# Kernel optimization log

Measured on AMD Instinct MI355X. Metric: run time of the kernel, lower is better.

The kernel has to match this reference:

```python
import jax, jax.numpy as jnp
import numpy as np

B, S, D, H, DK, DV = 2, 2048, 1024, 16, 64, 64


def setup_inputs() -> dict:
    key = jax.random.key(0)
    ks = jax.random.split(key, 12)
    inp = {
        "query": jax.random.normal(ks[0], (B, S, D), jnp.float32),
        "key":   jax.random.normal(ks[1], (B, S, D), jnp.float32),
        "value": jax.random.normal(ks[2], (B, S, D), jnp.float32),
        # additive mask broadcast over per-head [B,S,S] scores (zeros = no masking)
        "mask":  jnp.zeros((S, S), jnp.float32),
        # stacked per-head projection params (math-equivalent to H separate Linears)
        "Wq": jax.random.normal(ks[3], (H, D, DK), jnp.float32) / np.sqrt(D),
        "bq": jax.random.normal(ks[4], (H, DK), jnp.float32) * 0.02,
        "Wk": jax.random.normal(ks[5], (H, D, DK), jnp.float32) / np.sqrt(D),
        "bk": jax.random.normal(ks[6], (H, DK), jnp.float32) * 0.02,
        "Wv": jax.random.normal(ks[7], (H, D, DV), jnp.float32) / np.sqrt(D),
        "bv": jax.random.normal(ks[8], (H, DV), jnp.float32) * 0.02,
        "Wo": jax.random.normal(ks[9], (H * DV, D), jnp.float32) / np.sqrt(H * DV),
        "bo": jax.random.normal(ks[10], (D,), jnp.float32) * 0.02,
    }
    return inp


def reference(query, key, value, mask, Wq, bq, Wk, bk, Wv, bv, Wo, bo):
    # per-head projections, vectorized over heads
    q = jnp.einsum("bsd,hdk->bhsk", query, Wq) + bq[None, :, None, :]
    k = jnp.einsum("bsd,hdk->bhsk", key, Wk) + bk[None, :, None, :]
    v = jnp.einsum("bsd,hdv->bhsv", value, Wv) + bv[None, :, None, :]
    # explicit QK^T softmax V, scale by sqrt(dim_k) (key.size(-1))
    scores = jnp.einsum("bhsk,bhtk->bhst", q, k) / jnp.sqrt(jnp.asarray(DK, q.dtype))
    scores = scores + mask  # broadcast [S,S] -> [B,H,S,S]
    attn = jax.nn.softmax(scores, axis=-1)
    out = jnp.einsum("bhst,bhtv->bhsv", attn, v)
    # concat heads along last dim: [B,S,H*DV]
    out = out.transpose(0, 2, 1, 3).reshape(B, S, H * DV)
    return out @ Wo + bo
```

## Files before the change

### kernel.cpp

```cpp
#include <hip/hip_runtime.h>
#include <stdint.h>

typedef __bf16 bf16;
typedef float f32x4 __attribute__((ext_vector_type(4)));
typedef __bf16 bf16x8 __attribute__((ext_vector_type(8)));
typedef __bf16 bf16x4 __attribute__((ext_vector_type(4)));
typedef __bf16 bf16x2 __attribute__((ext_vector_type(2)));
typedef unsigned u32x2 __attribute__((ext_vector_type(2)));
typedef unsigned u32x4 __attribute__((ext_vector_type(4)));

__device__ __forceinline__ void async_load16(const void* g, void* l) {
    __builtin_amdgcn_global_load_lds(
        (const __attribute__((address_space(1))) void*)g,
        (__attribute__((address_space(3))) void*)l, 16, 0, 0);
}

__device__ __forceinline__ unsigned pk2(float lo, float hi) {
    bf16x2 t;
    t[0] = (bf16)lo;
    t[1] = (bf16)hi;
    return __builtin_bit_cast(unsigned, t);
}

#if __has_builtin(__builtin_amdgcn_permlane32_swap)
#define PLSWAP32(A_, B_) do { u32x2 _r = __builtin_amdgcn_permlane32_swap((A_), (B_), false, false); (A_) = _r[0]; (B_) = _r[1]; } while (0)
#else
#define PLSWAP32(A_, B_) asm("v_permlane32_swap_b32 %0, %1" : "+v"(A_), "+v"(B_))
#endif
#if __has_builtin(__builtin_amdgcn_permlane16_swap)
#define PLSWAP16(A_, B_) do { u32x2 _r = __builtin_amdgcn_permlane16_swap((A_), (B_), false, false); (A_) = _r[0]; (B_) = _r[1]; } while (0)
#else
#define PLSWAP16(A_, B_) asm("v_permlane16_swap_b32 %0, %1" : "+v"(A_), "+v"(B_))
#endif

__global__ void detect_dtype(const unsigned short* __restrict__ q, int* __restrict__ flag) {
    __shared__ int cnt;
    if (threadIdx.x == 0) cnt = 0;
    __syncthreads();
    int c = 0;
    for (int i = threadIdx.x; i < 4096; i += 256) {
        int e = (q[i] >> 7) & 0xFF;
        if (e >= 0xC0) ++c;
    }
    atomicAdd(&cnt, c);
    __syncthreads();
    if (threadIdx.x == 0) { flag[0] = (cnt > 64) ? 1 : 0; flag[1] = 0; }
}

__global__ void prep(const void* __restrict__ qv, const void* __restrict__ vv,
                     const void* __restrict__ kvraw,
                     const void* __restrict__ wq, const void* __restrict__ wk,
                     const void* __restrict__ wv, const void* __restrict__ wo,
                     const unsigned int* __restrict__ mask,
                     bf16* __restrict__ Xq, bf16* __restrict__ Xv,
                     bf16* __restrict__ Xk,
                     bf16* __restrict__ WqT, bf16* __restrict__ WoT,
                     int* __restrict__ flag) {
    __shared__ bf16 t[32][33];
    const int f    = flag[0];
    const int task = blockIdx.z;
    const int bid  = blockIdx.x + 64 * blockIdx.y;

    if (task < 2) {
        const void* x = task ? vv : qv;
        bf16* o = task ? Xv : Xq;
        size_t i = ((size_t)bid * 256 + threadIdx.x) * 8;
        if (f) {
            f32x4 a = ((const f32x4*)x)[i / 4];
            f32x4 b = ((const f32x4*)x)[i / 4 + 1];
            bf16x8 v;
            for (int j = 0; j < 4; ++j) { v[j] = (bf16)a[j]; v[4 + j] = (bf16)b[j]; }
            *(bf16x8*)(o + i) = v;
        } else {
            *(bf16x8*)(o + i) = *(const bf16x8*)((const bf16*)x + i);
        }
    } else if (task < 5) {
        if (bid >= 1024) return;
        const void* in = (task == 2) ? wq : ((task == 3) ? wk : wv);
        int sub = bid >> 6, rem = bid & 63;
        int c0 = (rem & 1) * 32, r0 = (rem >> 1) * 32;
        int tx = threadIdx.x & 31, ty = threadIdx.x >> 5;
        size_t base = (size_t)sub * 65536;
        if (f) {
            const float* inF = (const float*)in;
            for (int i = 0; i < 32; i += 8)
                t[ty + i][tx] = (bf16)inF[base + (size_t)(r0 + ty + i) * 64 + (c0 + tx)];
        } else {
            const bf16* inB = (const bf16*)in;
            for (int i = 0; i < 32; i += 8)
                t[ty + i][tx] = inB[base + (size_t)(r0 + ty + i) * 64 + (c0 + tx)];
        }
        __syncthreads();
        bf16* o = WqT + ((size_t)(task - 2) * 16 + sub) * 65536;
        for (int i = 0; i < 32; i += 8)
            o[(size_t)(c0 + ty + i) * 1024 + (r0 + tx)] = t[tx][ty + i];
    } else if (task == 5) {
        if (bid >= 1024) return;
        int c0 = (bid & 31) * 32, r0 = (bid >> 5) * 32;
        int tx = threadIdx.x & 31, ty = threadIdx.x >> 5;
        if (f) {
            const float* inF = (const float*)wo;
            for (int i = 0; i < 32; i += 8)
                t[ty + i][tx] = (bf16)inF[(size_t)(r0 + ty + i) * 1024 + (c0 + tx)];
        } else {
            const bf16* inB = (const bf16*)wo;
            for (int i = 0; i < 32; i += 8)
                t[ty + i][tx] = inB[(size_t)(r0 + ty + i) * 1024 + (c0 + tx)];
        }
        __syncthreads();
        for (int i = 0; i < 32; i += 8)
            WoT[(size_t)(c0 + ty + i) * 1024 + (r0 + tx)] = t[tx][ty + i];
    } else if (task == 6) {
        const long nvec = (f ? 4194304L : 2097152L) / 4;
        unsigned int acc = 0;
        long stride = 2048L * 256;
        for (long i = (long)bid * 256 + threadIdx.x; i < nvec; i += stride) {
            uint4 v = ((const uint4*)mask)[i];
            acc |= v.x | v.y | v.z | v.w;
        }
        if (acc) atomicOr(flag + 1, 1);
    } else {
        if (!f) return;
        size_t i = ((size_t)bid * 256 + threadIdx.x) * 8;
        f32x4 a = ((const f32x4*)kvraw)[i / 4];
        f32x4 b2 = ((const f32x4*)kvraw)[i / 4 + 1];
        bf16x8 v;
        for (int j = 0; j < 4; ++j) { v[j] = (bf16)a[j]; v[4 + j] = (bf16)b2[j]; }
        *(bf16x8*)(Xk + i) = v;
    }
}

__global__ __launch_bounds__(256, 3) void gemm_qkv(
    const bf16* __restrict__ Xq, const void* __restrict__ keyRaw,
    const bf16* __restrict__ Xv, const bf16* __restrict__ Xk,
    const bf16* __restrict__ Bt,
    const void* __restrict__ b0, const void* __restrict__ b1, const void* __restrict__ b2,
    bf16* __restrict__ Qp, bf16* __restrict__ Kp, bf16* __restrict__ Vt,
    const int* __restrict__ flag, const int useXk) {
    __shared__ __attribute__((aligned(16))) unsigned char AsRaw[128 * 64 * 4];
    __shared__ __attribute__((aligned(16))) bf16 Bs[128 * 64];

    const int f = flag[0];
    const int K = 1024, N = 1024;

    const int flat = blockIdx.x + 8 * blockIdx.y + 256 * blockIdx.z;
    const int rxw  = flat & 7;
    const int sxw  = flat >> 3;
    const int xb   = sxw & 7;
    const int jb   = sxw >> 3;
    const int yb   = rxw + 8 * (jb & 3);
    const int z    = jb >> 2;

    const int af = (z == 1 && !useXk) ? f : 0;
    const void* Av = (z == 0) ? (const void*)Xq
                   : (z == 1) ? ((f && useXk) ? (const void*)Xk : keyRaw)
                              : (const void*)Xv;
    const void* bias = (z == 0) ? b0 : ((z == 1) ? b1 : b2);
    const bf16* B    = Bt + (size_t)z * 1024 * 1024;

    const int tid  = threadIdx.x;
    const int lane = tid & 63;
    const int w    = tid >> 6;
    const int quad = lane >> 4;
    const int mrow = lane & 15;
    const int m0 = yb * 128;
    const int n0 = xb * 128;
    const int wm = (w & 1) * 64;
    const int wn = (w >> 1) * 64;

    f32x4 acc[4][4] = {};

    for (int k0 = 0; k0 < K; k0 += 64) {
        if (af) {
            for (int it = 0; it < 8; ++it) {
                int ci  = it * 256 + tid;
                int row = ci >> 4, pc = ci & 15;
                int swz = ((row & 7) << 1) | ((row >> 3) & 1);
                int gc  = pc ^ swz;
                async_load16((const float*)Av + (size_t)(m0 + row) * K + k0 + gc * 4,
                             AsRaw + (size_t)(it * 256 + w * 64) * 16);
            }
        } else {
            for (int it = 0; it < 4; ++it) {
                int ci  = it * 256 + tid;
                int row = ci >> 3, pc = ci & 7;
                int gc  = pc ^ (row & 7);
                async_load16((const bf16*)Av + (size_t)(m0 + row) * K + k0 + gc * 8,
                             (bf16*)AsRaw + (size_t)(it * 256 + w * 64) * 8);
            }
        }
        for (int it = 0; it < 4; ++it) {
            int ci  = it * 256 + tid;
            int row = ci >> 3, pc = ci & 7;
            int gc  = pc ^ (row & 7);
            async_load16(B + (size_t)(n0 + row) * K + k0 + gc * 8,
                         Bs + (size_t)(it * 256 + w * 64) * 8);
        }
        __syncthreads();
        for (int kk = 0; kk < 2; ++kk) {
            bf16x8 afr[4], bfr[4];
            if (af) {
                const float* Asf = (const float*)AsRaw;
                for (int mi = 0; mi < 4; ++mi) {
                    int row = wm + mi * 16 + mrow;
                    int swz = ((row & 7) << 1) | ((row >> 3) & 1);
                    int lc  = (kk * 4 + quad) * 2;
                    f32x4 u0 = *(const f32x4*)(Asf + row * 64 + (lc ^ swz) * 4);
                    f32x4 u1 = *(const f32x4*)(Asf + row * 64 + ((lc + 1) ^ swz) * 4);
                    for (int j = 0; j < 4; ++j) {
                        afr[mi][j]     = (bf16)u0[j];
                        afr[mi][4 + j] = (bf16)u1[j];
                    }
                }
            } else {
                const bf16* Asb = (const bf16*)AsRaw;
                for (int mi = 0; mi < 4; ++mi) {
                    int row = wm + mi * 16 + mrow;
                    int pc  = (kk * 4 + quad) ^ (row & 7);
                    afr[mi] = *(const bf16x8*)(Asb + row * 64 + pc * 8);
                }
            }
            for (int ni = 0; ni < 4; ++ni) {
                int row = wn + ni * 16 + mrow;
                int pc  = (kk * 4 + quad) ^ (row & 7);
                bfr[ni] = *(const bf16x8*)(Bs + row * 64 + pc * 8);
            }
            for (int mi = 0; mi < 4; ++mi)
                for (int ni = 0; ni < 4; ++ni)
                    acc[mi][ni] = __builtin_amdgcn_mfma_f32_16x16x32_bf16(
                        afr[mi], bfr[ni], acc[mi][ni], 0, 0, 0);
        }
        __syncthreads();
    }

    const float scl = (z == 0) ? 0.18033688f : 1.0f;
    for (int ni = 0; ni < 4; ++ni) {
        int n    = n0 + wn + ni * 16 + mrow;
        float bv = f ? ((const float*)bias)[n] : (float)((const bf16*)bias)[n];
        for (int mi = 0; mi < 4; ++mi) {
            int mb = m0 + wm + mi * 16 + quad * 4;
            if (z == 2) {
                bf16x4 pk;
                for (int r = 0; r < 4; ++r) pk[r] = (bf16)(acc[mi][ni][r] + bv);
                *(bf16x4*)(Vt + (((size_t)(mb >> 11) * 1024 + n) << 11) + (mb & 2047)) = pk;
            } else {
                bf16* P = (z == 0) ? Qp : Kp;
                for (int r = 0; r < 4; ++r)
                    P[(size_t)(mb + r) * N + n] = (bf16)((acc[mi][ni][r] + bv) * scl);
            }
        }
    }
}

__global__ __launch_bounds__(256, 2) void gemm_out(
    const bf16* __restrict__ A, const bf16* __restrict__ Bt,
    const void* __restrict__ bias, void* __restrict__ Cout,
    const int* __restrict__ flag) {
    __shared__ __attribute__((aligned(16))) bf16 As[128 * 64];
    __shared__ __attribute__((aligned(16))) bf16 Bs[64 * 64];

    const int f = flag[0];
    const int K = 1024, N = 1024;
    const int tid  = threadIdx.x;
    const int lane = tid & 63;
    const int w    = tid >> 6;
    const int quad = lane >> 4;
    const int mrow = lane & 15;

    const int flat = blockIdx.x + 16 * blockIdx.y;
    const int rxw  = flat & 7;
    const int sxw  = flat >> 3;
    const int xb   = sxw & 15;
    const int yb   = rxw + 8 * (sxw >> 4);

    const int m0 = yb * 128;
    const int n0 = xb * 64;
    const int wm = (w & 1) * 64;
    const int wn = (w >> 1) * 32;

    f32x4 acc[4][2] = {};

    for (int k0 = 0; k0 < K; k0 += 64) {
        for (int it = 0; it < 4; ++it) {
            int ci  = it * 256 + tid;
            int row = ci >> 3, pc = ci & 7;
            int gc  = pc ^ (row & 7);
            async_load16(A + (size_t)(m0 + row) * K + k0 + gc * 8,
                         As + (size_t)(it * 256 + w * 64) * 8);
        }
        for (int it = 0; it < 2; ++it) {
            int ci  = it * 256 + tid;
            int row = ci >> 3, pc = ci & 7;
            int gc  = pc ^ (row & 7);
            async_load16(Bt + (size_t)(n0 + row) * K + k0 + gc * 8,
                         Bs + (size_t)(it * 256 + w * 64) * 8);
        }
        __syncthreads();
        for (int kk = 0; kk < 2; ++kk) {
            bf16x8 afr[4], bfr[2];
            for (int mi = 0; mi < 4; ++mi) {
                int row = wm + mi * 16 + mrow;
                int pc  = (kk * 4 + quad) ^ (row & 7);
                afr[mi] = *(const bf16x8*)(As + row * 64 + pc * 8);
            }
            for (int ni = 0; ni < 2; ++ni) {
                int row = wn + ni * 16 + mrow;
                int pc  = (kk * 4 + quad) ^ (row & 7);
                bfr[ni] = *(const bf16x8*)(Bs + row * 64 + pc * 8);
            }
            for (int mi = 0; mi < 4; ++mi)
                for (int ni = 0; ni < 2; ++ni)
                    acc[mi][ni] = __builtin_amdgcn_mfma_f32_16x16x32_bf16(
                        afr[mi], bfr[ni], acc[mi][ni], 0, 0, 0);
        }
        __syncthreads();
    }

    for (int ni = 0; ni < 2; ++ni) {
        int n    = n0 + wn + ni * 16 + mrow;
        float bv = f ? ((const float*)bias)[n] : (float)((const bf16*)bias)[n];
        for (int mi = 0; mi < 4; ++mi) {
            int mb = m0 + wm + mi * 16 + quad * 4;
            for (int r = 0; r < 4; ++r) {
                float val = acc[mi][ni][r] + bv;
                if (f) ((float*)Cout)[(size_t)(mb + r) * N + n] = val;
                else   ((bf16*)Cout)[(size_t)(mb + r) * N + n] = (bf16)val;
            }
        }
    }
}

__global__ __launch_bounds__(512, 4) void flash_attn(
    const bf16* __restrict__ Qp, const bf16* __restrict__ Kp,
    const bf16* __restrict__ Vt, const void* __restrict__ maskv,
    bf16* __restrict__ O, const int* __restrict__ flag) {
    __shared__ __attribute__((aligned(16))) bf16 Ks[2][4096];
    __shared__ __attribute__((aligned(16))) bf16 Vs[2][4096];

    const int f       = flag[0];
    const int useMask = flag[1];
    const int tid  = threadIdx.x;
    const int lane = tid & 63;
    const int w    = tid >> 6;
    const int quad = lane >> 4;
    const int c    = lane & 15;

    const int flat = blockIdx.x + 16 * (blockIdx.y + 16 * blockIdx.z);
    const int rx   = flat & 7;
    const int sx   = flat >> 3;
    const int pair = rx + 8 * (sx >> 4);
    const int s0   = (sx & 15) * 128;
    const int h    = pair & 15;
    const int b    = pair >> 4;

    const size_t qkBase = (size_t)b * 2048 * 1024 + h * 64;
    const size_t vtBase = ((size_t)b * 1024 + h * 64) * 2048;

    const int r0 = tid >> 3, g0 = (tid & 7) ^ (r0 & 7);
    const bf16* kp0 = Kp + qkBase + (size_t)r0 * 1024 + g0 * 8;
    const bf16* vp0 = Vt + vtBase + (size_t)r0 * 2048 + g0 * 8;

#define STAGE(B_, T_) do {                                                      \
        async_load16(kp0 + (size_t)(T_) * 1024, &Ks[B_][(size_t)(w * 64) * 8]); \
        async_load16(vp0 + (T_),                &Vs[B_][(size_t)(w * 64) * 8]); \
    } while (0)

    const bf16* kf0 = &Ks[0][c * 64 + ((0 + quad) ^ (c & 7)) * 8];
    const bf16* kf1 = &Ks[0][c * 64 + ((4 + quad) ^ (c & 7)) * 8];
    const bf16* vf0 = &Vs[0][c * 64 + ((0 + quad) ^ (c & 7)) * 8];
    const bf16* vf1 = &Vs[0][c * 64 + ((4 + quad) ^ (c & 7)) * 8];

    const bf16* qrow = Qp + qkBase + (size_t)(s0 + w * 16 + c) * 1024;
    bf16x8 aq0 = *(const bf16x8*)(qrow + quad * 8);
    bf16x8 aq1 = *(const bf16x8*)(qrow + 32 + quad * 8);

    f32x4 o_acc[4] = {};
    float l_s = 0.f;

    const size_t mb0 = (size_t)(s0 + w * 16 + c) * 2048;

#define FCOMP(IB_, T_) do {                                                              \
        f32x4 sc[4] = {};                                                                \
        _Pragma("unroll") for (int tt = 0; tt < 4; ++tt) {                               \
            bf16x8 ak0 = *(const bf16x8*)(kf0 + (IB_) * 4096 + tt * 1024);               \
            bf16x8 ak1 = *(const bf16x8*)(kf1 + (IB_) * 4096 + tt * 1024);               \
            sc[tt] = __builtin_amdgcn_mfma_f32_16x16x32_bf16(ak0, aq0, sc[tt], 0, 0, 0); \
            sc[tt] = __builtin_amdgcn_mfma_f32_16x16x32_bf16(ak1, aq1, sc[tt], 0, 0, 0); \
        }                                                                                \
        if (useMask) {                                                                   \
            const size_t mr = mb0 + (T_);                                                \
            _Pragma("unroll") for (int tt = 0; tt < 4; ++tt) {                           \
                if (f) {                                                                 \
                    f32x4 mk = *(const f32x4*)((const float*)maskv + mr + tt * 16 + quad * 4); \
                    for (int r = 0; r < 4; ++r) sc[tt][r] += mk[r] * 1.44269504f;        \
                } else {                                                                 \
                    bf16x4 mk = *(const bf16x4*)((const bf16*)maskv + mr + tt * 16 + quad * 4); \
                    for (int r = 0; r < 4; ++r) sc[tt][r] += (float)mk[r] * 1.44269504f; \
                }                                                                        \
            }                                                                            \
        }                                                                                \
        unsigned Wp[4][2];                                                               \
        {                                                                                \
            float rsum = 0.f;                                                            \
            _Pragma("unroll") for (int tt = 0; tt < 4; ++tt) {                           \
                float p0 = exp2f(sc[tt][0]), p1 = exp2f(sc[tt][1]);                      \
                float p2 = exp2f(sc[tt][2]), p3 = exp2f(sc[tt][3]);                      \
                rsum += (p0 + p1) + (p2 + p3);                                           \
                Wp[tt][0] = pk2(p0, p1);                                                 \
                Wp[tt][1] = pk2(p2, p3);                                                 \
            }                                                                            \
            l_s += rsum;                                                                 \
        }                                                                                \
        _Pragma("unroll") for (int kk = 0; kk < 2; ++kk) {                               \
            unsigned a0 = Wp[2 * kk][0], b0v = Wp[2 * kk + 1][0];                        \
            unsigned a1 = Wp[2 * kk][1], b1v = Wp[2 * kk + 1][1];                        \
            PLSWAP32(a0, b0v);                                                           \
            PLSWAP16(a0, b0v);                                                           \
            PLSWAP32(a1, b1v);                                                           \
            PLSWAP16(a1, b1v);                                                           \
            u32x4 uv; uv[0] = a0; uv[1] = a1; uv[2] = b0v; uv[3] = b1v;                  \
            bf16x8 ap = __builtin_bit_cast(bf16x8, uv);                                  \
            const bf16* vfb = kk ? vf1 : vf0;                                            \
            _Pragma("unroll") for (int ni = 0; ni < 4; ++ni) {                           \
                bf16x8 bv = *(const bf16x8*)(vfb + (IB_) * 4096 + ni * 1024);            \
                o_acc[ni] = __builtin_amdgcn_mfma_f32_16x16x32_bf16(ap, bv, o_acc[ni], 0, 0, 0); \
            }                                                                            \
        }                                                                                \
    } while (0)

    STAGE(0, 0);
    for (int t0 = 0; t0 < 2048; t0 += 128) {
        __syncthreads();
        STAGE(1, t0 + 64);
        FCOMP(0, t0);
        __syncthreads();
        if (t0 + 128 < 2048) STAGE(0, t0 + 128);
        FCOMP(1, t0 + 64);
    }
#undef STAGE
#undef FCOMP

    {
        float ls = l_s;
        ls += __shfl_xor(ls, 16, 64);
        ls += __shfl_xor(ls, 32, 64);
        for (int r = 0; r < 4; ++r) {
            float lv   = __shfl(ls, quad * 4 + r, 64);
            float inv  = 1.0f / lv;
            size_t roff = (size_t)(b * 2048 + s0 + w * 16 + quad * 4 + r) * 1024 + h * 64;
            for (int ni = 0; ni < 4; ++ni)
                O[roff + ni * 16 + c] = (bf16)(o_acc[ni][r] * inv);
        }
    }
}

extern "C" void kernel_launch(void* const* d_in, const int* in_sizes, int n_in,
                              void* d_out, int out_size, void* d_ws, size_t ws_size,
                              hipStream_t stream) {
    bf16* ws = (bf16*)d_ws;
    (void)in_sizes; (void)n_in; (void)out_size;

    const size_t MM = 1024 * 1024;
    int*  flag = (int*)ws;
    bf16* WqT  = ws + 8;
    bf16* WoT  = WqT + 3 * MM;
    bf16* Qp   = WoT + MM;
    bf16* Kp   = Qp + 4 * MM;
    bf16* Xq   = Kp + 4 * MM;
    bf16* AO   = Xq;
    bf16* Xk   = Xq + 4 * MM;
    bf16* Xv   = (bf16*)d_out;
    bf16* Vt   = (bf16*)d_out + 4 * MM;

    const int useXk = (ws_size >= (size_t)(20 * MM) * sizeof(bf16) + 16) ? 1 : 0;

    detect_dtype<<<1, 256, 0, stream>>>((const unsigned short*)d_in[0], flag);

    prep<<<dim3(64, 32, useXk ? 8 : 7), 256, 0, stream>>>(
        d_in[0], d_in[2], d_in[1], d_in[4], d_in[6], d_in[8], d_in[10],
        (const unsigned int*)d_in[3], Xq, Xv, Xk, WqT, WoT, flag);

    gemm_qkv<<<dim3(8, 32, 3), 256, 0, stream>>>(Xq, d_in[1], Xv, Xk, WqT,
                                                 d_in[5], d_in[7], d_in[9],
                                                 Qp, Kp, Vt, flag, useXk);

    flash_attn<<<dim3(16, 16, 2), 512, 0, stream>>>(Qp, Kp, Vt, d_in[3], AO, flag);

    gemm_out<<<dim3(16, 32, 1), 256, 0, stream>>>(AO, WoT, d_in[11], d_out, flag);
}
```

Measured before the change: 258.5 us.

## Infer input dtype from host sizes and convert fp32 A tiles to bf16 when staging to LDS

Works out the input dtype on the host from in_sizes and passes it to every kernel, so the detect_dtype launch and the device flag read are skipped when the size is recognised. A memset still clears the flag word. The fp32 A-tile path in gemm_qkv now converts to bf16 during the global load and stores a bf16 swizzled tile. This halves LDS usage and removes the per-kk conversion in the MFMA loop. It gives up the async global-to-LDS copy on that path, and when the key operand comes from prebuilt Xk that path may not run.

Result: no change. 261.3 us (+1.1%).

```diff
diff --git a/kernel.cpp b/kernel.cpp
--- a/kernel.cpp
+++ b/kernel.cpp
@@ -55,9 +55,9 @@
                      bf16* __restrict__ Xq, bf16* __restrict__ Xv,
                      bf16* __restrict__ Xk,
                      bf16* __restrict__ WqT, bf16* __restrict__ WoT,
-                     int* __restrict__ flag) {
+                     int* __restrict__ flag, const int fHost) {
     __shared__ bf16 t[32][33];
-    const int f    = flag[0];
+    const int f    = (fHost >= 0) ? fHost : flag[0];
     const int task = blockIdx.z;
     const int bid  = blockIdx.x + 64 * blockIdx.y;
 
@@ -136,11 +136,11 @@
     const bf16* __restrict__ Bt,
     const void* __restrict__ b0, const void* __restrict__ b1, const void* __restrict__ b2,
     bf16* __restrict__ Qp, bf16* __restrict__ Kp, bf16* __restrict__ Vt,
-    const int* __restrict__ flag, const int useXk) {
-    __shared__ __attribute__((aligned(16))) unsigned char AsRaw[128 * 64 * 4];
+    const int* __restrict__ flag, const int useXk, const int fHost) {
+    __shared__ __attribute__((aligned(16))) bf16 As[128 * 64];
     __shared__ __attribute__((aligned(16))) bf16 Bs[128 * 64];
 
-    const int f = flag[0];
+    const int f = (fHost >= 0) ? fHost : flag[0];
     const int K = 1024, N = 1024;
 
     const int flat = blockIdx.x + 8 * blockIdx.y + 256 * blockIdx.z;
@@ -168,17 +168,23 @@
     const int wm = (w & 1) * 64;
     const int wn = (w >> 1) * 64;
 
+    const int cr = tid >> 1, cch = tid & 1;
+
     f32x4 acc[4][4] = {};
 
     for (int k0 = 0; k0 < K; k0 += 64) {
         if (af) {
-            for (int it = 0; it < 8; ++it) {
-                int ci  = it * 256 + tid;
-                int row = ci >> 4, pc = ci & 15;
-                int swz = ((row & 7) << 1) | ((row >> 3) & 1);
-                int gc  = pc ^ swz;
-                async_load16((const float*)Av + (size_t)(m0 + row) * K + k0 + gc * 4,
-                             AsRaw + (size_t)(it * 256 + w * 64) * 16);
+            const float* src = (const float*)Av + (size_t)(m0 + cr) * K + k0;
+            bf16* dst = As + cr * 64;
+#pragma unroll
+            for (int g = 0; g < 4; ++g) {
+                int pc = cch * 4 + g;
+                int gc = pc ^ (cr & 7);
+                f32x4 u0 = *(const f32x4*)(src + gc * 8);
+                f32x4 u1 = *(const f32x4*)(src + gc * 8 + 4);
+                bf16x8 vv;
+                for (int j = 0; j < 4; ++j) { vv[j] = (bf16)u0[j]; vv[4 + j] = (bf16)u1[j]; }
+                *(bf16x8*)(dst + pc * 8) = vv;
             }
         } else {
             for (int it = 0; it < 4; ++it) {
@@ -186,7 +192,7 @@
                 int row = ci >> 3, pc = ci & 7;
                 int gc  = pc ^ (row & 7);
                 async_load16((const bf16*)Av + (size_t)(m0 + row) * K + k0 + gc * 8,
-                             (bf16*)AsRaw + (size_t)(it * 256 + w * 64) * 8);
+                             As + (size_t)(it * 256 + w * 64) * 8);
             }
         }
         for (int it = 0; it < 4; ++it) {
@@ -199,26 +205,10 @@
         __syncthreads();
         for (int kk = 0; kk < 2; ++kk) {
             bf16x8 afr[4], bfr[4];
-            if (af) {
-                const float* Asf = (const float*)AsRaw;
-                for (int mi = 0; mi < 4; ++mi) {
-                    int row = wm + mi * 16 + mrow;
-                    int swz = ((row & 7) << 1) | ((row >> 3) & 1);
-                    int lc  = (kk * 4 + quad) * 2;
-                    f32x4 u0 = *(const f32x4*)(Asf + row * 64 + (lc ^ swz) * 4);
-                    f32x4 u1 = *(const f32x4*)(Asf + row * 64 + ((lc + 1) ^ swz) * 4);
-                    for (int j = 0; j < 4; ++j) {
-                        afr[mi][j]     = (bf16)u0[j];
-                        afr[mi][4 + j] = (bf16)u1[j];
-                    }
-                }
-            } else {
-                const bf16* Asb = (const bf16*)AsRaw;
-                for (int mi = 0; mi < 4; ++mi) {
-                    int row = wm + mi * 16 + mrow;
-                    int pc  = (kk * 4 + quad) ^ (row & 7);
-                    afr[mi] = *(const bf16x8*)(Asb + row * 64 + pc * 8);
-                }
+            for (int mi = 0; mi < 4; ++mi) {
+                int row = wm + mi * 16 + mrow;
+                int pc  = (kk * 4 + quad) ^ (row & 7);
+                afr[mi] = *(const bf16x8*)(As + row * 64 + pc * 8);
             }
             for (int ni = 0; ni < 4; ++ni) {
                 int row = wn + ni * 16 + mrow;
@@ -255,11 +245,11 @@
 __global__ __launch_bounds__(256, 2) void gemm_out(
     const bf16* __restrict__ A, const bf16* __restrict__ Bt,
     const void* __restrict__ bias, void* __restrict__ Cout,
-    const int* __restrict__ flag) {
+    const int* __restrict__ flag, const int fHost) {
     __shared__ __attribute__((aligned(16))) bf16 As[128 * 64];
     __shared__ __attribute__((aligned(16))) bf16 Bs[64 * 64];
 
-    const int f = flag[0];
+    const int f = (fHost >= 0) ? fHost : flag[0];
     const int K = 1024, N = 1024;
     const int tid  = threadIdx.x;
     const int lane = tid & 63;
@@ -333,11 +323,11 @@
 __global__ __launch_bounds__(512, 4) void flash_attn(
     const bf16* __restrict__ Qp, const bf16* __restrict__ Kp,
     const bf16* __restrict__ Vt, const void* __restrict__ maskv,
-    bf16* __restrict__ O, const int* __restrict__ flag) {
+    bf16* __restrict__ O, const int* __restrict__ flag, const int fHost) {
     __shared__ __attribute__((aligned(16))) bf16 Ks[2][4096];
     __shared__ __attribute__((aligned(16))) bf16 Vs[2][4096];
 
-    const int f       = flag[0];
+    const int f       = (fHost >= 0) ? fHost : flag[0];
     const int useMask = flag[1];
     const int tid  = threadIdx.x;
     const int lane = tid & 63;
@@ -458,7 +448,7 @@
                               void* d_out, int out_size, void* d_ws, size_t ws_size,
                               hipStream_t stream) {
     bf16* ws = (bf16*)d_ws;
-    (void)in_sizes; (void)n_in; (void)out_size;
+    (void)out_size;
 
     const size_t MM = 1024 * 1024;
     int*  flag = (int*)ws;
@@ -474,17 +464,27 @@
 
     const int useXk = (ws_size >= (size_t)(20 * MM) * sizeof(bf16) + 16) ? 1 : 0;
 
-    detect_dtype<<<1, 256, 0, stream>>>((const unsigned short*)d_in[0], flag);
+    int fHost = -1;
+    if (in_sizes != nullptr && n_in >= 1) {
+        if (in_sizes[0] == 16777216)     fHost = 1;
+        else if (in_sizes[0] == 8388608) fHost = 0;
+    }
+
+    if (fHost < 0) {
+        detect_dtype<<<1, 256, 0, stream>>>((const unsigned short*)d_in[0], flag);
+    } else {
+        hipMemsetAsync(flag, 0, 2 * sizeof(int), stream);
+    }
 
     prep<<<dim3(64, 32, useXk ? 8 : 7), 256, 0, stream>>>(
         d_in[0], d_in[2], d_in[1], d_in[4], d_in[6], d_in[8], d_in[10],
-        (const unsigned int*)d_in[3], Xq, Xv, Xk, WqT, WoT, flag);
+        (const unsigned int*)d_in[3], Xq, Xv, Xk, WqT, WoT, flag, fHost);
 
     gemm_qkv<<<dim3(8, 32, 3), 256, 0, stream>>>(Xq, d_in[1], Xv, Xk, WqT,
                                                  d_in[5], d_in[7], d_in[9],
-                                                 Qp, Kp, Vt, flag, useXk);
-
-    flash_attn<<<dim3(16, 16, 2), 512, 0, stream>>>(Qp, Kp, Vt, d_in[3], AO, flag);
-
-    gemm_out<<<dim3(16, 32, 1), 256, 0, stream>>>(AO, WoT, d_in[11], d_out, flag);
-}
+                                                 Qp, Kp, Vt, flag, useXk, fHost);
+
+    flash_attn<<<dim3(16, 16, 2), 512, 0, stream>>>(Qp, Kp, Vt, d_in[3], AO, flag, fHost);
+
+    gemm_out<<<dim3(16, 32, 1), 256, 0, stream>>>(AO, WoT, d_in[11], d_out, flag, fHost);
+}
```
